# Kernel optimization log

Measured on AMD Instinct MI355X. Metric: run time of the kernel, lower is better.

Reference implementation:

```python
import jax, jax.numpy as jnp
import numpy as np
import math

SQRT2 = float(np.sqrt(2.0))
INV_SQRT_2PI = float(1.0 / np.sqrt(2.0 * np.pi))


def _trunc_prob(x, mu, sigma):
    # Faithful port of TruncNormal.prob with a=-10, b=10
    a, b = -10.0, 10.0
    phi_b = 0.5 * (1.0 + jax.scipy.special.erf((b - mu) / sigma / SQRT2))
    phi_a = 0.5 * (1.0 + jax.scipy.special.erf((a - mu) / sigma / SQRT2))
    xs = jnp.where(x > b, x + 100.0, x)
    xs = jnp.where(xs < a, xs - 100.0, xs)
    xn = (xs - mu) / sigma
    dens = jnp.exp(-0.5 * xn * xn) * INV_SQRT_2PI
    dens = jnp.where((xn > b) | (xn < a), 0.0, dens)
    return dens / (phi_b - phi_a) + 1e-10


def _S_single(zg, tt, Wx, bx, Wt, bt, Wt2, bt2, Wf, bf, Wo, bo):
    # One tiny MLP applied to one group-slice zg (shape [g]) at scalar time tt.
    g = Wx.shape[0]
    x = jnp.tanh(Wx @ zg + bx)
    half = g // 2
    freqs = jnp.exp(jnp.arange(half, dtype=zg.dtype) * (-math.log(10000.0) / half))
    te = tt * freqs
    temb = jnp.concatenate([jnp.sin(te), jnp.cos(te)])  # [g]
    tv = jax.nn.gelu(Wt @ temb + bt, approximate=False)  # torch nn.GELU (exact)
    tv = Wt2 @ tv + bt2
    h = jnp.tanh(Wf @ (x + tv) + bf)
    return jnp.tanh(Wo @ h + bo)[0]  # scalar S


def _derivs(zg, tt, Wx, bx, Wt, bt, Wt2, bt2, Wf, bf, Wo, bo):
    p = (Wx, bx, Wt, bt, Wt2, bt2, Wf, bf, Wo, bo)
    f = lambda z_, t_: _S_single(z_, t_, *p)
    S = f(zg, tt)
    s_z = jax.grad(f, 0)(zg, tt)                    # dS/dz         [g]
    H = jax.jacfwd(jax.grad(f, 0), 0)(zg, tt)       # H[j,k]=d2S/dzj dzk  [g,g]
    dSdt = jax.grad(f, 1)(zg, tt)                   # dS/dt scalar
    return S, s_z, H, dSdt


def reference(z, time_step, mu, sigma, Wx, bx, Wt, bt, Wt2, bt2, Wf, bf, Wo, bo, beta):
    G, g = Wx.shape[0], Wx.shape[1]
    B = z.shape[0]
    tt = time_step[0]

    sig2 = sigma ** 2 + 1e-5
    nlp = -(z - mu) / sig2                                   # nabla_log_phi [B,n_in]
    dlp = -1.0 / sig2                                        # delta_log_phi (scalar-ish)
    dpp = ((z - mu) ** 2 - sigma ** 2) / (sigma ** 4 + 1e-5)  # delta_phi_over_phi
    rho = _trunc_prob(z, mu, sigma)

    to_g = lambda a: a.reshape(B, G, g).transpose(1, 0, 2)   # [G,B,g]
    zr, nlp_r, dpp_r, rho_r = to_g(z), to_g(nlp), to_g(dpp), to_g(rho)

    over_b = jax.vmap(_derivs, in_axes=(0, None) + (None,) * 10)
    over_g = jax.vmap(over_b, in_axes=(0, None) + (0,) * 10)
    S, s_z, H, dSdt = over_g(zr, tt, Wx, bx, Wt, bt, Wt2, bt2, Wf, bf, Wo, bo)
    # S [G,B], s_z [G,B,g], H [G,B,g,g], dSdt [G,B]

    bb = beta.reshape(G, 1, 1)
    u = S[..., None] - bb * jnp.log(jnp.prod(rho_r, axis=2, keepdims=True))  # [G,B,1]
    u_z = s_z - bb * nlp_r                                                    # [G,B,g]
    # torch grad(S.sum(), t): t is a single shared (1,1) tensor -> gradient sums over batch
    dSdt_sum = dSdt.sum(axis=1).reshape(G, 1, 1)
    # grad((rho*u_z).sum(), z_temp): rho and nabla_log_phi are constants wrt z_temp,
    # so gradient = sum_j rho_j * H[j,k]
    corr = jnp.einsum('gbj,gbjk->gbk', rho_r, H)
    u_t = dSdt_sum + bb * corr / (rho_r + 1e-5)
    # grad(s_z.sum(), z_temp)[k] = sum_j H[j,k]
    u_zz = H.sum(axis=2) - bb * dlp
    pde = u_t + 0.5 * u_z ** 2 + 0.125 * bb ** 2 * (nlp_r ** 2 - 2.0 * dpp_r)

    to_bn = lambda a: a.transpose(1, 0, 2).reshape(B, -1)
    return to_bn(pde), to_bn(u_z), u[:, :, 0].transpose(1, 0), to_bn(u_zz)


def setup_inputs() -> dict:
    B, N_IN, g = 8192, 512, 4
    G = N_IN // g
    key = jax.random.key(0)
    ks = jax.random.split(key, 16)

    def lin_w(k, fo, fi):
        return (jax.random.normal(k, (G, fo, fi), jnp.float32) / np.sqrt(fi)).astype(jnp.float32)

    def lin_b(k, fo):
        return (0.01 * jax.random.normal(k, (G, fo), jnp.float32)).astype(jnp.float32)

    return {
        "z": jax.random.normal(ks[0], (B, N_IN), jnp.float32),
        "time_step": jnp.ones((1,), jnp.float32),
        "mu": jnp.zeros((1,), jnp.float32),
        "sigma": jnp.ones((1,), jnp.float32),
        "Wx": lin_w(ks[1], g, g), "bx": lin_b(ks[2], g),
        "Wt": lin_w(ks[3], g, g), "bt": lin_b(ks[4], g),
        "Wt2": lin_w(ks[5], g, g), "bt2": lin_b(ks[6], g),
        "Wf": lin_w(ks[7], g, g), "bf": lin_b(ks[8], g),
        "Wo": lin_w(ks[9], 1, g), "bo": lin_b(ks[10], 1),
        "beta": jnp.ones((G, 1), jnp.float32),
    }
```

## Files before the change

### kernel.cpp

```cpp
#include <hip/hip_runtime.h>
#include <math.h>

#define NG 128
#define NIN 512
#define OFF1 4194304
#define OFF2 8388608
#define OFF3 9437184

#define INV_SQRT_2PI 0.3989422804014327f
#define INV_SQRT2    0.7071067811865476f

typedef float f32x4 __attribute__((ext_vector_type(4)));

__device__ __forceinline__ float ftanh(float x){
    float e = __expf(2.0f*x);
    float r = __builtin_amdgcn_rcpf(e + 1.0f);
    return 1.0f - 2.0f*r;
}
__device__ __forceinline__ float frcp(float x){ return __builtin_amdgcn_rcpf(x); }

__device__ __forceinline__ float gelu_f(float x){
    return 0.5f*x*(1.0f + erff(x*INV_SQRT2));
}
__device__ __forceinline__ float gelu_df(float x){
    return 0.5f*(1.0f + erff(x*INV_SQRT2)) + x*INV_SQRT_2PI*__expf(-0.5f*x*x);
}

__global__ void k_pre(const float* __restrict__ ts,
                      const float* __restrict__ mup, const float* __restrict__ sigp,
                      const float* __restrict__ Wt,  const float* __restrict__ bt,
                      const float* __restrict__ Wt2, const float* __restrict__ bt2,
                      float* __restrict__ tv_ws, float* __restrict__ dtv_ws,
                      float* __restrict__ consts){
    int g = threadIdx.x;
    if (g == 0){
        float mu = mup[0], sigma = sigp[0];
        float sig2  = sigma*sigma + 1e-5f;
        float phi_b = 0.5f*(1.0f+erff((10.0f-mu)/sigma*INV_SQRT2));
        float phi_a = 0.5f*(1.0f+erff((-10.0f-mu)/sigma*INV_SQRT2));
        consts[0] = sig2;
        consts[1] = -1.0f/sig2;
        consts[2] = 1.0f/(sigma*sigma*sigma*sigma + 1e-5f);
        consts[3] = 1.0f/(phi_b-phi_a);
        consts[4] = mu;
        consts[5] = 1.0f/sigma;
        consts[6] = sigma;
    }
    if (g >= NG) return;
    float t  = ts[0];
    const float f1 = 0.01f;
    float s0, c0, s1, c1;
    __sincosf(t, &s0, &c0);
    __sincosf(t*f1, &s1, &c1);
    float temb[4]  = { s0, s1, c0, c1 };
    float dtemb[4] = { c0, f1*c1, -s0, -f1*s1 };
    float tg[4], dg[4];
    #pragma unroll
    for (int i=0;i<4;i++){
        float a = bt[g*4+i], d = 0.0f;
        #pragma unroll
        for (int j=0;j<4;j++){
            float w = Wt[g*16+i*4+j];
            a += w*temb[j]; d += w*dtemb[j];
        }
        tg[i] = gelu_f(a);
        dg[i] = gelu_df(a)*d;
    }
    #pragma unroll
    for (int j=0;j<4;j++){
        float a = bt2[g*4+j], d = 0.0f;
        #pragma unroll
        for (int i=0;i<4;i++){
            float w = Wt2[g*16+j*4+i];
            a += w*tg[i]; d += w*dg[i];
        }
        tv_ws[g*4+j]  = a;
        dtv_ws[g*4+j] = d;
    }
}

__global__ __launch_bounds__(256) void k_dsdt(const float* __restrict__ z,
    const float* __restrict__ Wx, const float* __restrict__ bx,
    const float* __restrict__ Wf, const float* __restrict__ bf,
    const float* __restrict__ Wo, const float* __restrict__ bo,
    const float* __restrict__ tv_ws, const float* __restrict__ dtv_ws,
    float* __restrict__ partial){
    const int tid  = threadIdx.x;
    const int gidx = tid & 127;
    const int lb   = tid >> 7;
    float wx[16], wf[16];
    #pragma unroll
    for (int i=0;i<4;i++){
        float4 a4 = ((const float4*)(Wx + gidx*16))[i];
        wx[i*4+0]=a4.x; wx[i*4+1]=a4.y; wx[i*4+2]=a4.z; wx[i*4+3]=a4.w;
        float4 b4 = ((const float4*)(Wf + gidx*16))[i];
        wf[i*4+0]=b4.x; wf[i*4+1]=b4.y; wf[i*4+2]=b4.z; wf[i*4+3]=b4.w;
    }
    float4 t4;
    t4 = ((const float4*)bx)[gidx];     float bxA[4]={t4.x,t4.y,t4.z,t4.w};
    t4 = ((const float4*)bf)[gidx];     float bfA[4]={t4.x,t4.y,t4.z,t4.w};
    t4 = ((const float4*)Wo)[gidx];     float w3[4] ={t4.x,t4.y,t4.z,t4.w};
    t4 = ((const float4*)tv_ws)[gidx];  float tvA[4]={t4.x,t4.y,t4.z,t4.w};
    t4 = ((const float4*)dtv_ws)[gidx]; float dtvA[4]={t4.x,t4.y,t4.z,t4.w};
    const float bo0 = bo[gidx];

    const int r0 = blockIdx.x*8 + lb*4;

    float zz[4][4];
    #pragma unroll
    for (int r=0;r<4;r++){
        float4 zv = *((const float4*)(z + (r0+r)*NIN + gidx*4));
        zz[r][0]=zv.x; zz[r][1]=zv.y; zz[r][2]=zv.z; zz[r][3]=zv.w;
    }
    float u1[4][4];
    #pragma unroll
    for (int r=0;r<4;r++){
        #pragma unroll
        for (int i=0;i<4;i++){
            float a = bxA[i] + wx[i*4]*zz[r][0]+wx[i*4+1]*zz[r][1]
                             + wx[i*4+2]*zz[r][2]+wx[i*4+3]*zz[r][3];
            u1[r][i] = ftanh(a) + tvA[i];
        }
    }
    float hp[4][4], a3[4];
    #pragma unroll
    for (int r=0;r<4;r++) a3[r] = bo0;
    #pragma unroll
    for (int r=0;r<4;r++){
        #pragma unroll
        for (int i=0;i<4;i++){
            float a = bfA[i] + wf[i*4]*u1[r][0]+wf[i*4+1]*u1[r][1]
                             + wf[i*4+2]*u1[r][2]+wf[i*4+3]*u1[r][3];
            float h = ftanh(a);
            hp[r][i] = 1.0f - h*h;
            a3[r] += w3[i]*h;
        }
    }
    float acc = 0.0f;
    #pragma unroll
    for (int r=0;r<4;r++){
        float S = ftanh(a3[r]), sp = 1.0f - S*S;
        float q0=0,q1=0,q2=0,q3=0;
        #pragma unroll
        for (int i=0;i<4;i++){
            float vi = sp*w3[i]*hp[r][i];
            q0 += vi*wf[i*4+0]; q1 += vi*wf[i*4+1];
            q2 += vi*wf[i*4+2]; q3 += vi*wf[i*4+3];
        }
        acc += q0*dtvA[0]+q1*dtvA[1]+q2*dtvA[2]+q3*dtvA[3];
    }

    __shared__ float sred[256];
    sred[tid] = acc;
    __syncthreads();
    if (tid < 128) partial[blockIdx.x*128 + tid] = sred[tid] + sred[tid+128];
}

__global__ __launch_bounds__(256) void k_red(const float* __restrict__ partial,
                                             float* __restrict__ dsum){
    int g = blockIdx.x;
    int tid = threadIdx.x;
    float a = 0.0f;
    for (int i=tid;i<1024;i+=256) a += partial[i*128+g];
    __shared__ float s[256];
    s[tid] = a;
    __syncthreads();
    if (tid < 64){
        a = s[tid] + s[tid+64] + s[tid+128] + s[tid+192];
        #pragma unroll
        for (int o=32;o>0;o>>=1) a += __shfl_down(a, o);
        if (tid==0) dsum[g] = a;
    }
}

__global__ __launch_bounds__(256) void k_main(const float* __restrict__ z,
    const float* __restrict__ Wx, const float* __restrict__ bx,
    const float* __restrict__ Wf, const float* __restrict__ bf,
    const float* __restrict__ Wo, const float* __restrict__ bo,
    const float* __restrict__ betap, const float* __restrict__ tv_ws,
    const float* __restrict__ consts,
    const float* __restrict__ dsum, float* __restrict__ out){
    const int tid  = threadIdx.x;
    const int gidx = tid & 127;
    const int row0 = blockIdx.x*4 + (tid>>7)*2;

    const float sig2    = consts[0];
    const float dlp     = consts[1];
    const float inv_s4  = consts[2];
    const float invZ    = consts[3];
    const float mu      = consts[4];
    const float inv_sig = consts[5];
    const float sigma   = consts[6];
    const float inv_sig2 = frcp(sig2);

    float wx[16], wf[16];
    #pragma unroll
    for (int i=0;i<4;i++){
        float4 a4 = ((const float4*)(Wx + gidx*16))[i];
        wx[i*4+0]=a4.x; wx[i*4+1]=a4.y; wx[i*4+2]=a4.z; wx[i*4+3]=a4.w;
        float4 b4 = ((const float4*)(Wf + gidx*16))[i];
        wf[i*4+0]=b4.x; wf[i*4+1]=b4.y; wf[i*4+2]=b4.z; wf[i*4+3]=b4.w;
    }
    float4 t4;
    t4 = ((const float4*)bx)[gidx];    float bxA[4]={t4.x,t4.y,t4.z,t4.w};
    t4 = ((const float4*)bf)[gidx];    float bfA[4]={t4.x,t4.y,t4.z,t4.w};
    t4 = ((const float4*)Wo)[gidx];    float w3[4] ={t4.x,t4.y,t4.z,t4.w};
    t4 = ((const float4*)tv_ws)[gidx]; float tvA[4]={t4.x,t4.y,t4.z,t4.w};
    const float bo0    = bo[gidx];
    const float bb     = betap[gidx];
    const float dS_sum = dsum[gidx];

    float zz[2][4], x_[2][4], xp[2][4], h_[2][4], hp[2][4], S[2], sp[2], q[2][4];
    #pragma unroll
    for (int r=0;r<2;r++){
        float4 zv = *((const float4*)(z + (row0+r)*NIN + gidx*4));
        zz[r][0]=zv.x; zz[r][1]=zv.y; zz[r][2]=zv.z; zz[r][3]=zv.w;
    }
    float u1[2][4];
    #pragma unroll
    for (int r=0;r<2;r++){
        #pragma unroll
        for (int i=0;i<4;i++){
            float a = bxA[i] + wx[i*4]*zz[r][0]+wx[i*4+1]*zz[r][1]
                             + wx[i*4+2]*zz[r][2]+wx[i*4+3]*zz[r][3];
            x_[r][i] = ftanh(a);
        }
    }
    #pragma unroll
    for (int r=0;r<2;r++){
        #pragma unroll
        for (int i=0;i<4;i++){
            xp[r][i] = 1.0f - x_[r][i]*x_[r][i];
            u1[r][i] = x_[r][i] + tvA[i];
        }
    }
    float a3[2] = { bo0, bo0 };
    #pragma unroll
    for (int r=0;r<2;r++){
        #pragma unroll
        for (int i=0;i<4;i++){
            float a = bfA[i] + wf[i*4]*u1[r][0]+wf[i*4+1]*u1[r][1]
                             + wf[i*4+2]*u1[r][2]+wf[i*4+3]*u1[r][3];
            h_[r][i] = ftanh(a);
        }
    }
    #pragma unroll
    for (int r=0;r<2;r++){
        #pragma unroll
        for (int i=0;i<4;i++){
            hp[r][i] = 1.0f - h_[r][i]*h_[r][i];
            a3[r] += w3[i]*h_[r][i];
        }
    }
    #pragma unroll
    for (int r=0;r<2;r++){ S[r] = ftanh(a3[r]); sp[r] = 1.0f - S[r]*S[r]; }
    #pragma unroll
    for (int r=0;r<2;r++){
        q[r][0]=q[r][1]=q[r][2]=q[r][3]=0.0f;
        #pragma unroll
        for (int i=0;i<4;i++){
            float vi = sp[r]*w3[i]*hp[r][i];
            #pragma unroll
            for (int j=0;j<4;j++) q[r][j] += vi*wf[i*4+j];
        }
    }

    #pragma unroll
    for (int r=0;r<2;r++){
        float Bm[16];
        #pragma unroll
        for (int i=0;i<4;i++){
            #pragma unroll
            for (int n=0;n<4;n++){
                float s = 0.0f;
                #pragma unroll
                for (int k=0;k<4;k++) s += wf[i*4+k]*xp[r][k]*wx[k*4+n];
                Bm[i*4+n]=s;
            }
        }
        float w3hp[4], v[4];
        #pragma unroll
        for (int i=0;i<4;i++){ w3hp[i]=w3[i]*hp[r][i]; v[i]=sp[r]*w3hp[i]; }
        float c[4];
        #pragma unroll
        for (int n=0;n<4;n++){
            float s=0.0f;
            #pragma unroll
            for (int i=0;i<4;i++) s += w3hp[i]*Bm[i*4+n];
            c[n]=s;
        }
        const float alpha = -2.0f*S[r]*sp[r];
        float bet[4], gam[4];
        #pragma unroll
        for (int i=0;i<4;i++){
            bet[i] = -2.0f*h_[r][i]*v[i];
            gam[i] = -2.0f*x_[r][i]*xp[r][i]*q[r][i];
        }

        float rho[4], nlp[4], dpp[4];
        #pragma unroll
        for (int j=0;j<4;j++){
            float zj = zz[r][j];
            float xs = zj > 10.0f ? zj+100.0f : zj;
            xs = xs < -10.0f ? xs-100.0f : xs;
            float xn = (xs-mu)*inv_sig;
            float dens = __expf(-0.5f*xn*xn)*INV_SQRT_2PI;
            dens = (xn > 10.0f || xn < -10.0f) ? 0.0f : dens;
            rho[j] = dens*invZ + 1e-10f;
            nlp[j] = -(zj-mu)*inv_sig2;
            float d = zj-mu;
            dpp[j] = (d*d - sigma*sigma)*inv_s4;
        }
        float u_val = S[r] - bb*__logf(rho[0]*rho[1]*rho[2]*rho[3]);

        float rc=0.0f, scs=0.0f;
        #pragma unroll
        for (int j=0;j<4;j++){ rc += rho[j]*c[j]; scs += c[j]; }
        float rB[4], sB[4], rA[4], sA[4];
        #pragma unroll
        for (int i=0;i<4;i++){
            float r1=0.0f, s=0.0f, r2=0.0f, s2=0.0f;
            #pragma unroll
            for (int j=0;j<4;j++){
                r1 += rho[j]*Bm[i*4+j]; s  += Bm[i*4+j];
                r2 += rho[j]*wx[i*4+j]; s2 += wx[i*4+j];
            }
            rB[i]=r1; sB[i]=s; rA[i]=r2; sA[i]=s2;
        }

        float pde[4], uz[4], uzz[4];
        #pragma unroll
        for (int k=0;k<4;k++){
            float corr = alpha*rc*c[k];
            float hsum = alpha*scs*c[k];
            #pragma unroll
            for (int i=0;i<4;i++){
                corr += bet[i]*rB[i]*Bm[i*4+k];
                hsum += bet[i]*sB[i]*Bm[i*4+k];
                corr += gam[i]*rA[i]*wx[i*4+k];
                hsum += gam[i]*sA[i]*wx[i*4+k];
            }
            float uzk = sp[r]*c[k] - bb*nlp[k];
            uz[k]  = uzk;
            uzz[k] = hsum - bb*dlp;
            pde[k] = dS_sum + bb*corr*frcp(rho[k]+1e-5f)
                   + 0.5f*uzk*uzk + 0.125f*bb*bb*(nlp[k]*nlp[k] - 2.0f*dpp[k]);
        }

        const int base = (row0+r)*NIN + gidx*4;
        f32x4 pdev = { pde[0], pde[1], pde[2], pde[3] };
        f32x4 uzv  = { uz[0],  uz[1],  uz[2],  uz[3]  };
        f32x4 uzzv = { uzz[0], uzz[1], uzz[2], uzz[3] };
        __builtin_nontemporal_store(pdev, (f32x4*)(out + base));
        __builtin_nontemporal_store(uzv,  (f32x4*)(out + OFF1 + base));
        __builtin_nontemporal_store(u_val, out + OFF2 + (row0+r)*NG + gidx);
        __builtin_nontemporal_store(uzzv, (f32x4*)(out + OFF3 + base));
    }
}

extern "C" void kernel_launch(void* const* d_in, const int* in_sizes, int n_in,
                              void* d_out, int out_size, void* d_ws, size_t ws_size,
                              hipStream_t stream){
    (void)in_sizes; (void)n_in; (void)out_size; (void)ws_size;
    const float* z     = (const float*)d_in[0];
    const float* ts    = (const float*)d_in[1];
    const float* mu    = (const float*)d_in[2];
    const float* sigma = (const float*)d_in[3];
    const float* Wx    = (const float*)d_in[4];
    const float* bx    = (const float*)d_in[5];
    const float* Wt    = (const float*)d_in[6];
    const float* bt    = (const float*)d_in[7];
    const float* Wt2   = (const float*)d_in[8];
    const float* bt2   = (const float*)d_in[9];
    const float* Wf    = (const float*)d_in[10];
    const float* bf    = (const float*)d_in[11];
    const float* Wo    = (const float*)d_in[12];
    const float* bo    = (const float*)d_in[13];
    const float* beta  = (const float*)d_in[14];
    float* out = (float*)d_out;

    float* ws      = (float*)d_ws;
    float* tv_ws   = ws;
    float* dtv_ws  = ws + 512;
    float* consts  = ws + 1024;
    float* dsum    = ws + 1032;
    float* partial = ws + 1160;

    k_pre <<<1,   128, 0, stream>>>(ts, mu, sigma, Wt, bt, Wt2, bt2,
                                    tv_ws, dtv_ws, consts);
    k_dsdt<<<1024,256, 0, stream>>>(z, Wx, bx, Wf, bf, Wo, bo, tv_ws, dtv_ws, partial);
    k_red <<<128, 256, 0, stream>>>(partial, dsum);
    k_main<<<2048,256, 0, stream>>>(z, Wx, bx, Wf, bf, Wo, bo, beta, tv_ws,
                                    consts, dsum, out);
}
```

Measured before the change: 126.5 us.

## Fuse dS/dt reduction into main kernel and add dsum afterwards in fixup pass

```diff
diff --git a/kernel.cpp b/kernel.cpp
--- a/kernel.cpp
+++ b/kernel.cpp
@@ -26,68 +26,65 @@
     return 0.5f*(1.0f + erff(x*INV_SQRT2)) + x*INV_SQRT_2PI*__expf(-0.5f*x*x);
 }
 
-__global__ void k_pre(const float* __restrict__ ts,
-                      const float* __restrict__ mup, const float* __restrict__ sigp,
-                      const float* __restrict__ Wt,  const float* __restrict__ bt,
-                      const float* __restrict__ Wt2, const float* __restrict__ bt2,
-                      float* __restrict__ tv_ws, float* __restrict__ dtv_ws,
-                      float* __restrict__ consts){
-    int g = threadIdx.x;
-    if (g == 0){
-        float mu = mup[0], sigma = sigp[0];
-        float sig2  = sigma*sigma + 1e-5f;
-        float phi_b = 0.5f*(1.0f+erff((10.0f-mu)/sigma*INV_SQRT2));
-        float phi_a = 0.5f*(1.0f+erff((-10.0f-mu)/sigma*INV_SQRT2));
-        consts[0] = sig2;
-        consts[1] = -1.0f/sig2;
-        consts[2] = 1.0f/(sigma*sigma*sigma*sigma + 1e-5f);
-        consts[3] = 1.0f/(phi_b-phi_a);
-        consts[4] = mu;
-        consts[5] = 1.0f/sigma;
-        consts[6] = sigma;
-    }
-    if (g >= NG) return;
-    float t  = ts[0];
-    const float f1 = 0.01f;
-    float s0, c0, s1, c1;
-    __sincosf(t, &s0, &c0);
-    __sincosf(t*f1, &s1, &c1);
-    float temb[4]  = { s0, s1, c0, c1 };
-    float dtemb[4] = { c0, f1*c1, -s0, -f1*s1 };
-    float tg[4], dg[4];
-    #pragma unroll
-    for (int i=0;i<4;i++){
-        float a = bt[g*4+i], d = 0.0f;
-        #pragma unroll
-        for (int j=0;j<4;j++){
-            float w = Wt[g*16+i*4+j];
-            a += w*temb[j]; d += w*dtemb[j];
-        }
-        tg[i] = gelu_f(a);
-        dg[i] = gelu_df(a)*d;
-    }
-    #pragma unroll
-    for (int j=0;j<4;j++){
-        float a = bt2[g*4+j], d = 0.0f;
-        #pragma unroll
-        for (int i=0;i<4;i++){
-            float w = Wt2[g*16+j*4+i];
-            a += w*tg[i]; d += w*dg[i];
-        }
-        tv_ws[g*4+j]  = a;
-        dtv_ws[g*4+j] = d;
-    }
-}
-
-__global__ __launch_bounds__(256) void k_dsdt(const float* __restrict__ z,
+__global__ __launch_bounds__(256) void k_all(const float* __restrict__ z,
     const float* __restrict__ Wx, const float* __restrict__ bx,
     const float* __restrict__ Wf, const float* __restrict__ bf,
     const float* __restrict__ Wo, const float* __restrict__ bo,
-    const float* __restrict__ tv_ws, const float* __restrict__ dtv_ws,
-    float* __restrict__ partial){
+    const float* __restrict__ betap,
+    const float* __restrict__ ts, const float* __restrict__ mup,
+    const float* __restrict__ sigp,
+    const float* __restrict__ Wt, const float* __restrict__ bt,
+    const float* __restrict__ Wt2, const float* __restrict__ bt2,
+    float* __restrict__ partial, float* __restrict__ out){
     const int tid  = threadIdx.x;
     const int gidx = tid & 127;
-    const int lb   = tid >> 7;
+    const int row0 = blockIdx.x*4 + (tid>>7)*2;
+
+    const float t     = ts[0];
+    const float mu    = mup[0];
+    const float sigma = sigp[0];
+    const float sig2    = sigma*sigma + 1e-5f;
+    const float dlp     = -1.0f/sig2;
+    const float inv_s4  = 1.0f/(sigma*sigma*sigma*sigma + 1e-5f);
+    const float phi_b   = 0.5f*(1.0f+erff((10.0f-mu)/sigma*INV_SQRT2));
+    const float phi_a   = 0.5f*(1.0f+erff((-10.0f-mu)/sigma*INV_SQRT2));
+    const float invZ    = 1.0f/(phi_b-phi_a);
+    const float inv_sig = 1.0f/sigma;
+    const float inv_sig2 = frcp(sig2);
+
+    float tvA[4], dtvA[4];
+    {
+        const float f1 = 0.01f;
+        float s0, c0, s1, c1;
+        __sincosf(t, &s0, &c0);
+        __sincosf(t*f1, &s1, &c1);
+        float temb[4]  = { s0, s1, c0, c1 };
+        float dtemb[4] = { c0, f1*c1, -s0, -f1*s1 };
+        float tg[4], dg[4];
+        #pragma unroll
+        for (int i=0;i<4;i++){
+            float a = bt[gidx*4+i], d = 0.0f;
+            #pragma unroll
+            for (int j=0;j<4;j++){
+                float w = Wt[gidx*16+i*4+j];
+                a += w*temb[j]; d += w*dtemb[j];
+            }
+            tg[i] = gelu_f(a);
+            dg[i] = gelu_df(a)*d;
+        }
+        #pragma unroll
+        for (int j=0;j<4;j++){
+            float a = bt2[gidx*4+j], d = 0.0f;
+            #pragma unroll
+            for (int i=0;i<4;i++){
+                float w = Wt2[gidx*16+j*4+i];
+                a += w*tg[i]; d += w*dg[i];
+            }
+            tvA[j]  = a;
+            dtvA[j] = d;
+        }
+    }
+
     float wx[16], wf[16];
     #pragma unroll
     for (int i=0;i<4;i++){
@@ -97,118 +94,11 @@
         wf[i*4+0]=b4.x; wf[i*4+1]=b4.y; wf[i*4+2]=b4.z; wf[i*4+3]=b4.w;
     }
     float4 t4;
-    t4 = ((const float4*)bx)[gidx];     float bxA[4]={t4.x,t4.y,t4.z,t4.w};
-    t4 = ((const float4*)bf)[gidx];     float bfA[4]={t4.x,t4.y,t4.z,t4.w};
-    t4 = ((const float4*)Wo)[gidx];     float w3[4] ={t4.x,t4.y,t4.z,t4.w};
-    t4 = ((const float4*)tv_ws)[gidx];  float tvA[4]={t4.x,t4.y,t4.z,t4.w};
-    t4 = ((const float4*)dtv_ws)[gidx]; float dtvA[4]={t4.x,t4.y,t4.z,t4.w};
-    const float bo0 = bo[gidx];
-
-    const int r0 = blockIdx.x*8 + lb*4;
-
-    float zz[4][4];
-    #pragma unroll
-    for (int r=0;r<4;r++){
-        float4 zv = *((const float4*)(z + (r0+r)*NIN + gidx*4));
-        zz[r][0]=zv.x; zz[r][1]=zv.y; zz[r][2]=zv.z; zz[r][3]=zv.w;
-    }
-    float u1[4][4];
-    #pragma unroll
-    for (int r=0;r<4;r++){
-        #pragma unroll
-        for (int i=0;i<4;i++){
-            float a = bxA[i] + wx[i*4]*zz[r][0]+wx[i*4+1]*zz[r][1]
-                             + wx[i*4+2]*zz[r][2]+wx[i*4+3]*zz[r][3];
-            u1[r][i] = ftanh(a) + tvA[i];
-        }
-    }
-    float hp[4][4], a3[4];
-    #pragma unroll
-    for (int r=0;r<4;r++) a3[r] = bo0;
-    #pragma unroll
-    for (int r=0;r<4;r++){
-        #pragma unroll
-        for (int i=0;i<4;i++){
-            float a = bfA[i] + wf[i*4]*u1[r][0]+wf[i*4+1]*u1[r][1]
-                             + wf[i*4+2]*u1[r][2]+wf[i*4+3]*u1[r][3];
-            float h = ftanh(a);
-            hp[r][i] = 1.0f - h*h;
-            a3[r] += w3[i]*h;
-        }
-    }
-    float acc = 0.0f;
-    #pragma unroll
-    for (int r=0;r<4;r++){
-        float S = ftanh(a3[r]), sp = 1.0f - S*S;
-        float q0=0,q1=0,q2=0,q3=0;
-        #pragma unroll
-        for (int i=0;i<4;i++){
-            float vi = sp*w3[i]*hp[r][i];
-            q0 += vi*wf[i*4+0]; q1 += vi*wf[i*4+1];
-            q2 += vi*wf[i*4+2]; q3 += vi*wf[i*4+3];
-        }
-        acc += q0*dtvA[0]+q1*dtvA[1]+q2*dtvA[2]+q3*dtvA[3];
-    }
-
-    __shared__ float sred[256];
-    sred[tid] = acc;
-    __syncthreads();
-    if (tid < 128) partial[blockIdx.x*128 + tid] = sred[tid] + sred[tid+128];
-}
-
-__global__ __launch_bounds__(256) void k_red(const float* __restrict__ partial,
-                                             float* __restrict__ dsum){
-    int g = blockIdx.x;
-    int tid = threadIdx.x;
-    float a = 0.0f;
-    for (int i=tid;i<1024;i+=256) a += partial[i*128+g];
-    __shared__ float s[256];
-    s[tid] = a;
-    __syncthreads();
-    if (tid < 64){
-        a = s[tid] + s[tid+64] + s[tid+128] + s[tid+192];
-        #pragma unroll
-        for (int o=32;o>0;o>>=1) a += __shfl_down(a, o);
-        if (tid==0) dsum[g] = a;
-    }
-}
-
-__global__ __launch_bounds__(256) void k_main(const float* __restrict__ z,
-    const float* __restrict__ Wx, const float* __restrict__ bx,
-    const float* __restrict__ Wf, const float* __restrict__ bf,
-    const float* __restrict__ Wo, const float* __restrict__ bo,
-    const float* __restrict__ betap, const float* __restrict__ tv_ws,
-    const float* __restrict__ consts,
-    const float* __restrict__ dsum, float* __restrict__ out){
-    const int tid  = threadIdx.x;
-    const int gidx = tid & 127;
-    const int row0 = blockIdx.x*4 + (tid>>7)*2;
-
-    const float sig2    = consts[0];
-    const float dlp     = consts[1];
-    const float inv_s4  = consts[2];
-    const float invZ    = consts[3];
-    const float mu      = consts[4];
-    const float inv_sig = consts[5];
-    const float sigma   = consts[6];
-    const float inv_sig2 = frcp(sig2);
-
-    float wx[16], wf[16];
-    #pragma unroll
-    for (int i=0;i<4;i++){
-        float4 a4 = ((const float4*)(Wx + gidx*16))[i];
-        wx[i*4+0]=a4.x; wx[i*4+1]=a4.y; wx[i*4+2]=a4.z; wx[i*4+3]=a4.w;
-        float4 b4 = ((const float4*)(Wf + gidx*16))[i];
-        wf[i*4+0]=b4.x; wf[i*4+1]=b4.y; wf[i*4+2]=b4.z; wf[i*4+3]=b4.w;
-    }
-    float4 t4;
     t4 = ((const float4*)bx)[gidx];    float bxA[4]={t4.x,t4.y,t4.z,t4.w};
     t4 = ((const float4*)bf)[gidx];    float bfA[4]={t4.x,t4.y,t4.z,t4.w};
     t4 = ((const float4*)Wo)[gidx];    float w3[4] ={t4.x,t4.y,t4.z,t4.w};
-    t4 = ((const float4*)tv_ws)[gidx]; float tvA[4]={t4.x,t4.y,t4.z,t4.w};
-    const float bo0    = bo[gidx];
-    const float bb     = betap[gidx];
-    const float dS_sum = dsum[gidx];
+    const float bo0 = bo[gidx];
+    const float bb  = betap[gidx];
 
     float zz[2][4], x_[2][4], xp[2][4], h_[2][4], hp[2][4], S[2], sp[2], q[2][4];
     #pragma unroll
@@ -264,6 +154,9 @@
             for (int j=0;j<4;j++) q[r][j] += vi*wf[i*4+j];
         }
     }
+
+    float accd = q[0][0]*dtvA[0]+q[0][1]*dtvA[1]+q[0][2]*dtvA[2]+q[0][3]*dtvA[3]
+               + q[1][0]*dtvA[0]+q[1][1]*dtvA[1]+q[1][2]*dtvA[2]+q[1][3]*dtvA[3];
 
     #pragma unroll
     for (int r=0;r<2;r++){
@@ -343,7 +236,7 @@
             float uzk = sp[r]*c[k] - bb*nlp[k];
             uz[k]  = uzk;
             uzz[k] = hsum - bb*dlp;
-            pde[k] = dS_sum + bb*corr*frcp(rho[k]+1e-5f)
+            pde[k] = bb*corr*frcp(rho[k]+1e-5f)
                    + 0.5f*uzk*uzk + 0.125f*bb*bb*(nlp[k]*nlp[k] - 2.0f*dpp[k]);
         }
 
@@ -351,11 +244,47 @@
         f32x4 pdev = { pde[0], pde[1], pde[2], pde[3] };
         f32x4 uzv  = { uz[0],  uz[1],  uz[2],  uz[3]  };
         f32x4 uzzv = { uzz[0], uzz[1], uzz[2], uzz[3] };
-        __builtin_nontemporal_store(pdev, (f32x4*)(out + base));
+        *((f32x4*)(out + base)) = pdev;
         __builtin_nontemporal_store(uzv,  (f32x4*)(out + OFF1 + base));
         __builtin_nontemporal_store(u_val, out + OFF2 + (row0+r)*NG + gidx);
         __builtin_nontemporal_store(uzzv, (f32x4*)(out + OFF3 + base));
     }
+
+    __shared__ float sred[256];
+    sred[tid] = accd;
+    __syncthreads();
+    if (tid < 128) partial[blockIdx.x*128 + tid] = sred[tid] + sred[tid+128];
+}
+
+__global__ __launch_bounds__(256) void k_red(const float* __restrict__ partial,
+                                             float* __restrict__ dsum){
+    int g = blockIdx.x;
+    int tid = threadIdx.x;
+    float a = 0.0f;
+    for (int i=tid;i<2048;i+=256) a += partial[i*128+g];
+    __shared__ float s[256];
+    s[tid] = a;
+    __syncthreads();
+    if (tid < 64){
+        a = s[tid] + s[tid+64] + s[tid+128] + s[tid+192];
+        #pragma unroll
+        for (int o=32;o>0;o>>=1) a += __shfl_down(a, o);
+        if (tid==0) dsum[g] = a;
+    }
+}
+
+__global__ __launch_bounds__(256) void k_fix(const float* __restrict__ dsum,
+                                             float* __restrict__ out){
+    const int idx = blockIdx.x*256 + threadIdx.x;
+    const float ds = dsum[idx & 127];
+    f32x4* p = (f32x4*)out;
+    f32x4 v = p[idx];
+    v.x += ds; v.y += ds; v.z += ds; v.w += ds;
+    p[idx] = v;
+    const int idx2 = idx + 524288;
+    f32x4 w = p[idx2];
+    w.x += ds; w.y += ds; w.z += ds; w.w += ds;
+    p[idx2] = w;
 }
 
 extern "C" void kernel_launch(void* const* d_in, const int* in_sizes, int n_in,
@@ -380,16 +309,12 @@
     float* out = (float*)d_out;
 
     float* ws      = (float*)d_ws;
-    float* tv_ws   = ws;
-    float* dtv_ws  = ws + 512;
-    float* consts  = ws + 1024;
-    float* dsum    = ws + 1032;
-    float* partial = ws + 1160;
-
-    k_pre <<<1,   128, 0, stream>>>(ts, mu, sigma, Wt, bt, Wt2, bt2,
-                                    tv_ws, dtv_ws, consts);
-    k_dsdt<<<1024,256, 0, stream>>>(z, Wx, bx, Wf, bf, Wo, bo, tv_ws, dtv_ws, partial);
-    k_red <<<128, 256, 0, stream>>>(partial, dsum);
-    k_main<<<2048,256, 0, stream>>>(z, Wx, bx, Wf, bf, Wo, bo, beta, tv_ws,
-                                    consts, dsum, out);
-}
+    float* dsum    = ws;
+    float* partial = ws + 128;
+
+    k_all<<<2048,256, 0, stream>>>(z, Wx, bx, Wf, bf, Wo, bo, beta,
+                                   ts, mu, sigma, Wt, bt, Wt2, bt2,
+                                   partial, out);
+    k_red<<<128, 256, 0, stream>>>(partial, dsum);
+    k_fix<<<2048,256, 0, stream>>>(dsum, out);
+}
```

New measurement: 137.8 us. +9.0%, slower.

## Fuse pre/dsdt/reduce/main into one cooperative kernel with grid syncs

Applied to the files above, without the earlier changes.

```diff
diff --git a/kernel.cpp b/kernel.cpp
--- a/kernel.cpp
+++ b/kernel.cpp
@@ -1,5 +1,8 @@
 #include <hip/hip_runtime.h>
+#include <hip/hip_cooperative_groups.h>
 #include <math.h>
+
+namespace cg = cooperative_groups;
 
 #define NG 128
 #define NIN 512
@@ -24,6 +27,285 @@
 }
 __device__ __forceinline__ float gelu_df(float x){
     return 0.5f*(1.0f + erff(x*INV_SQRT2)) + x*INV_SQRT_2PI*__expf(-0.5f*x*x);
+}
+
+__global__ __launch_bounds__(256, 2) void k_coop(const float* __restrict__ z,
+    const float* __restrict__ Wx, const float* __restrict__ bx,
+    const float* __restrict__ Wf, const float* __restrict__ bf,
+    const float* __restrict__ Wo, const float* __restrict__ bo,
+    const float* __restrict__ betap,
+    const float* __restrict__ ts, const float* __restrict__ mup,
+    const float* __restrict__ sigp,
+    const float* __restrict__ Wt, const float* __restrict__ bt,
+    const float* __restrict__ Wt2, const float* __restrict__ bt2,
+    float* __restrict__ partial, float* __restrict__ dsum,
+    float* __restrict__ out){
+
+    __shared__ float st[8*16*128];
+    __shared__ float sred[256];
+
+    const int tid  = threadIdx.x;
+    const int gidx = tid & 127;
+    const int slot = tid >> 7;
+    const int rs0  = slot*8;
+    const int R0   = blockIdx.x*16 + slot*8;
+
+    float zz[8][4];
+    #pragma unroll
+    for (int r=0;r<8;r++){
+        float4 zv = *((const float4*)(z + (R0+r)*NIN + gidx*4));
+        zz[r][0]=zv.x; zz[r][1]=zv.y; zz[r][2]=zv.z; zz[r][3]=zv.w;
+    }
+
+    float wx[16], wf[16];
+    #pragma unroll
+    for (int i=0;i<4;i++){
+        float4 a4 = ((const float4*)(Wx + gidx*16))[i];
+        wx[i*4+0]=a4.x; wx[i*4+1]=a4.y; wx[i*4+2]=a4.z; wx[i*4+3]=a4.w;
+        float4 b4 = ((const float4*)(Wf + gidx*16))[i];
+        wf[i*4+0]=b4.x; wf[i*4+1]=b4.y; wf[i*4+2]=b4.z; wf[i*4+3]=b4.w;
+    }
+    float4 t4;
+    t4 = ((const float4*)bx)[gidx];    float bxA[4]={t4.x,t4.y,t4.z,t4.w};
+    t4 = ((const float4*)bf)[gidx];    float bfA[4]={t4.x,t4.y,t4.z,t4.w};
+    t4 = ((const float4*)Wo)[gidx];    float w3[4] ={t4.x,t4.y,t4.z,t4.w};
+    const float bo0 = bo[gidx];
+    const float bb  = betap[gidx];
+
+    const float t     = ts[0];
+    const float mu    = mup[0];
+    const float sigma = sigp[0];
+    const float sig2    = sigma*sigma + 1e-5f;
+    const float dlp     = -1.0f/sig2;
+    const float inv_s4  = 1.0f/(sigma*sigma*sigma*sigma + 1e-5f);
+    const float phi_b   = 0.5f*(1.0f+erff((10.0f-mu)/sigma*INV_SQRT2));
+    const float phi_a   = 0.5f*(1.0f+erff((-10.0f-mu)/sigma*INV_SQRT2));
+    const float invZ    = 1.0f/(phi_b-phi_a);
+    const float inv_sig = 1.0f/sigma;
+    const float inv_sig2 = frcp(sig2);
+
+    float tvA[4], wfdtv[4];
+    {
+        const float f1 = 0.01f;
+        float s0, c0, s1, c1;
+        __sincosf(t, &s0, &c0);
+        __sincosf(t*f1, &s1, &c1);
+        float temb[4]  = { s0, s1, c0, c1 };
+        float dtemb[4] = { c0, f1*c1, -s0, -f1*s1 };
+        float tg[4], dg[4];
+        #pragma unroll
+        for (int i=0;i<4;i++){
+            float a = bt[gidx*4+i], d = 0.0f;
+            #pragma unroll
+            for (int j=0;j<4;j++){
+                float w = Wt[gidx*16+i*4+j];
+                a += w*temb[j]; d += w*dtemb[j];
+            }
+            tg[i] = gelu_f(a);
+            dg[i] = gelu_df(a)*d;
+        }
+        float dtvA[4];
+        #pragma unroll
+        for (int j=0;j<4;j++){
+            float a = bt2[gidx*4+j], d = 0.0f;
+            #pragma unroll
+            for (int i=0;i<4;i++){
+                float w = Wt2[gidx*16+j*4+i];
+                a += w*tg[i]; d += w*dg[i];
+            }
+            tvA[j]  = a;
+            dtvA[j] = d;
+        }
+        #pragma unroll
+        for (int i=0;i<4;i++)
+            wfdtv[i] = wf[i*4]*dtvA[0]+wf[i*4+1]*dtvA[1]
+                     + wf[i*4+2]*dtvA[2]+wf[i*4+3]*dtvA[3];
+    }
+
+    float accd = 0.0f;
+    #pragma unroll
+    for (int p=0;p<4;p++){
+        const int ra = 2*p, rb = 2*p+1;
+        float x0[4], x1[4];
+        #pragma unroll
+        for (int i=0;i<4;i++){
+            float a0 = bxA[i] + wx[i*4]*zz[ra][0]+wx[i*4+1]*zz[ra][1]
+                              + wx[i*4+2]*zz[ra][2]+wx[i*4+3]*zz[ra][3];
+            float a1 = bxA[i] + wx[i*4]*zz[rb][0]+wx[i*4+1]*zz[rb][1]
+                              + wx[i*4+2]*zz[rb][2]+wx[i*4+3]*zz[rb][3];
+            x0[i] = ftanh(a0); x1[i] = ftanh(a1);
+        }
+        float u10[4], u11[4];
+        #pragma unroll
+        for (int i=0;i<4;i++){ u10[i]=x0[i]+tvA[i]; u11[i]=x1[i]+tvA[i]; }
+        float h0[4], h1[4];
+        float a30 = bo0, a31 = bo0;
+        #pragma unroll
+        for (int i=0;i<4;i++){
+            float a0 = bfA[i] + wf[i*4]*u10[0]+wf[i*4+1]*u10[1]
+                              + wf[i*4+2]*u10[2]+wf[i*4+3]*u10[3];
+            float a1 = bfA[i] + wf[i*4]*u11[0]+wf[i*4+1]*u11[1]
+                              + wf[i*4+2]*u11[2]+wf[i*4+3]*u11[3];
+            h0[i] = ftanh(a0); h1[i] = ftanh(a1);
+        }
+        #pragma unroll
+        for (int i=0;i<4;i++){ a30 += w3[i]*h0[i]; a31 += w3[i]*h1[i]; }
+        float S0 = ftanh(a30), S1 = ftanh(a31);
+        float sp0 = 1.0f - S0*S0, sp1 = 1.0f - S1*S1;
+        #pragma unroll
+        for (int i=0;i<4;i++){
+            accd += sp0*w3[i]*(1.0f-h0[i]*h0[i])*wfdtv[i]
+                  + sp1*w3[i]*(1.0f-h1[i]*h1[i])*wfdtv[i];
+        }
+        const int ba = (rs0+ra)*128 + gidx;
+        const int bb2 = (rs0+rb)*128 + gidx;
+        #pragma unroll
+        for (int i=0;i<4;i++){
+            st[(i*16)*128 + ba]      = x0[i];
+            st[(i*16)*128 + bb2]     = x1[i];
+            st[((4+i)*16)*128 + ba]  = h0[i];
+            st[((4+i)*16)*128 + bb2] = h1[i];
+        }
+    }
+
+    sred[tid] = accd;
+    __syncthreads();
+    if (tid < 128) partial[blockIdx.x*128 + tid] = sred[tid] + sred[tid+128];
+
+    cg::this_grid().sync();
+
+    if (blockIdx.x < 128){
+        const int g = blockIdx.x;
+        float a = partial[(2*tid)*128 + g] + partial[(2*tid+1)*128 + g];
+        sred[tid] = a;
+        __syncthreads();
+        if (tid < 64){
+            a = sred[tid] + sred[tid+64] + sred[tid+128] + sred[tid+192];
+            #pragma unroll
+            for (int o=32;o>0;o>>=1) a += __shfl_down(a, o);
+            if (tid == 0) dsum[g] = a;
+        }
+    }
+
+    cg::this_grid().sync();
+
+    const float dS_sum = dsum[gidx];
+    #pragma unroll 2
+    for (int r=0;r<8;r++){
+        const int bi = (rs0+r)*128 + gidx;
+        float x_[4], h_[4];
+        #pragma unroll
+        for (int i=0;i<4;i++){
+            x_[i] = st[(i*16)*128 + bi];
+            h_[i] = st[((4+i)*16)*128 + bi];
+        }
+        float xp[4], hp[4];
+        float a3 = bo0;
+        #pragma unroll
+        for (int i=0;i<4;i++){
+            xp[i] = 1.0f - x_[i]*x_[i];
+            hp[i] = 1.0f - h_[i]*h_[i];
+            a3 += w3[i]*h_[i];
+        }
+        const float S  = ftanh(a3);
+        const float sp = 1.0f - S*S;
+        float q[4] = {0,0,0,0};
+        #pragma unroll
+        for (int i=0;i<4;i++){
+            float vi = sp*w3[i]*hp[i];
+            #pragma unroll
+            for (int j=0;j<4;j++) q[j] += vi*wf[i*4+j];
+        }
+
+        float Bm[16];
+        #pragma unroll
+        for (int i=0;i<4;i++){
+            #pragma unroll
+            for (int n=0;n<4;n++){
+                float s = 0.0f;
+                #pragma unroll
+                for (int k=0;k<4;k++) s += wf[i*4+k]*xp[k]*wx[k*4+n];
+                Bm[i*4+n]=s;
+            }
+        }
+        float w3hp[4], v[4];
+        #pragma unroll
+        for (int i=0;i<4;i++){ w3hp[i]=w3[i]*hp[i]; v[i]=sp*w3hp[i]; }
+        float c[4];
+        #pragma unroll
+        for (int n=0;n<4;n++){
+            float s=0.0f;
+            #pragma unroll
+            for (int i=0;i<4;i++) s += w3hp[i]*Bm[i*4+n];
+            c[n]=s;
+        }
+        const float alpha = -2.0f*S*sp;
+        float bet[4], gam[4];
+        #pragma unroll
+        for (int i=0;i<4;i++){
+            bet[i] = -2.0f*h_[i]*v[i];
+            gam[i] = -2.0f*x_[i]*xp[i]*q[i];
+        }
+
+        float rho[4], nlp[4], dpp[4];
+        #pragma unroll
+        for (int j=0;j<4;j++){
+            float zj = zz[r][j];
+            float xs = zj > 10.0f ? zj+100.0f : zj;
+            xs = xs < -10.0f ? xs-100.0f : xs;
+            float xn = (xs-mu)*inv_sig;
+            float dens = __expf(-0.5f*xn*xn)*INV_SQRT_2PI;
+            dens = (xn > 10.0f || xn < -10.0f) ? 0.0f : dens;
+            rho[j] = dens*invZ + 1e-10f;
+            nlp[j] = -(zj-mu)*inv_sig2;
+            float d = zj-mu;
+            dpp[j] = (d*d - sigma*sigma)*inv_s4;
+        }
+        float u_val = S - bb*__logf(rho[0]*rho[1]*rho[2]*rho[3]);
+
+        float rc=0.0f, scs=0.0f;
+        #pragma unroll
+        for (int j=0;j<4;j++){ rc += rho[j]*c[j]; scs += c[j]; }
+        float rB[4], sB[4], rA[4], sA[4];
+        #pragma unroll
+        for (int i=0;i<4;i++){
+            float r1=0.0f, s=0.0f, r2=0.0f, s2=0.0f;
+            #pragma unroll
+            for (int j=0;j<4;j++){
+                r1 += rho[j]*Bm[i*4+j]; s  += Bm[i*4+j];
+                r2 += rho[j]*wx[i*4+j]; s2 += wx[i*4+j];
+            }
+            rB[i]=r1; sB[i]=s; rA[i]=r2; sA[i]=s2;
+        }
+
+        float pde[4], uz[4], uzz[4];
+        #pragma unroll
+        for (int k=0;k<4;k++){
+            float corr = alpha*rc*c[k];
+            float hsum = alpha*scs*c[k];
+            #pragma unroll
+            for (int i=0;i<4;i++){
+                corr += bet[i]*rB[i]*Bm[i*4+k];
+                hsum += bet[i]*sB[i]*Bm[i*4+k];
+                corr += gam[i]*rA[i]*wx[i*4+k];
+                hsum += gam[i]*sA[i]*wx[i*4+k];
+            }
+            float uzk = sp*c[k] - bb*nlp[k];
+            uz[k]  = uzk;
+            uzz[k] = hsum - bb*dlp;
+            pde[k] = dS_sum + bb*corr*frcp(rho[k]+1e-5f)
+                   + 0.5f*uzk*uzk + 0.125f*bb*bb*(nlp[k]*nlp[k] - 2.0f*dpp[k]);
+        }
+
+        const int base = (R0+r)*NIN + gidx*4;
+        f32x4 pdev = { pde[0], pde[1], pde[2], pde[3] };
+        f32x4 uzv  = { uz[0],  uz[1],  uz[2],  uz[3]  };
+        f32x4 uzzv = { uzz[0], uzz[1], uzz[2], uzz[3] };
+        __builtin_nontemporal_store(pdev, (f32x4*)(out + base));
+        __builtin_nontemporal_store(uzv,  (f32x4*)(out + OFF1 + base));
+        __builtin_nontemporal_store(u_val, out + OFF2 + (R0+r)*NG + gidx);
+        __builtin_nontemporal_store(uzzv, (f32x4*)(out + OFF3 + base));
+    }
 }
 
 __global__ void k_pre(const float* __restrict__ ts,
@@ -156,8 +438,8 @@
     if (tid < 128) partial[blockIdx.x*128 + tid] = sred[tid] + sred[tid+128];
 }
 
-__global__ __launch_bounds__(256) void k_red(const float* __restrict__ partial,
-                                             float* __restrict__ dsum){
+__global__ __launch_bounds__(256) void k_redf(const float* __restrict__ partial,
+                                              float* __restrict__ dsum){
     int g = blockIdx.x;
     int tid = threadIdx.x;
     float a = 0.0f;
@@ -380,16 +662,36 @@
     float* out = (float*)d_out;
 
     float* ws      = (float*)d_ws;
-    float* tv_ws   = ws;
-    float* dtv_ws  = ws + 512;
-    float* consts  = ws + 1024;
-    float* dsum    = ws + 1032;
-    float* partial = ws + 1160;
-
-    k_pre <<<1,   128, 0, stream>>>(ts, mu, sigma, Wt, bt, Wt2, bt2,
-                                    tv_ws, dtv_ws, consts);
-    k_dsdt<<<1024,256, 0, stream>>>(z, Wx, bx, Wf, bf, Wo, bo, tv_ws, dtv_ws, partial);
-    k_red <<<128, 256, 0, stream>>>(partial, dsum);
-    k_main<<<2048,256, 0, stream>>>(z, Wx, bx, Wf, bf, Wo, bo, beta, tv_ws,
-                                    consts, dsum, out);
-}
+    float* dsum    = ws;
+    float* partial = ws + 128;
+    float* fws      = ws + 100000;
+    float* tv_ws    = fws;
+    float* dtv_ws   = fws + 512;
+    float* consts   = fws + 1024;
+    float* fdsum    = fws + 1032;
+    float* fpartial = fws + 1160;
+
+    const float* a_z = z;   const float* a_Wx = Wx;  const float* a_bx = bx;
+    const float* a_Wf = Wf; const float* a_bf = bf;  const float* a_Wo = Wo;
+    const float* a_bo = bo; const float* a_beta = beta;
+    const float* a_ts = ts; const float* a_mu = mu;  const float* a_sig = sigma;
+    const float* a_Wt = Wt; const float* a_bt = bt;
+    const float* a_Wt2 = Wt2; const float* a_bt2 = bt2;
+    float* a_partial = partial; float* a_dsum = dsum; float* a_out = out;
+    void* args[] = { &a_z, &a_Wx, &a_bx, &a_Wf, &a_bf, &a_Wo, &a_bo, &a_beta,
+                     &a_ts, &a_mu, &a_sig, &a_Wt, &a_bt, &a_Wt2, &a_bt2,
+                     &a_partial, &a_dsum, &a_out };
+
+    hipError_t e = hipLaunchCooperativeKernel((const void*)k_coop,
+                                              dim3(512), dim3(256),
+                                              args, 0, stream);
+    if (e != hipSuccess){
+        k_pre <<<1,   128, 0, stream>>>(ts, mu, sigma, Wt, bt, Wt2, bt2,
+                                        tv_ws, dtv_ws, consts);
+        k_dsdt<<<1024,256, 0, stream>>>(z, Wx, bx, Wf, bf, Wo, bo,
+                                        tv_ws, dtv_ws, fpartial);
+        k_redf<<<128, 256, 0, stream>>>(fpartial, fdsum);
+        k_main<<<2048,256, 0, stream>>>(z, Wx, bx, Wf, bf, Wo, bo, beta, tv_ws,
+                                        consts, fdsum, out);
+    }
+}
```

Result: slower. 245.8 us (+94.4%).
